# Performance work log

Hardware: AMD Instinct MI355X
Metric: run time of the kernel (lower is better)

## Reference

```python
import jax, jax.numpy as jnp
import numpy as np

N, E, D, G, L = 100_000, 500_000, 128, 512, 4
BN_EPS = 1e-5

def _bn(v, g, b):
    # BatchNorm1d in training mode: biased batch stats over node/graph axis
    m = v.mean(0)
    var = v.var(0)
    return (v - m) * jax.lax.rsqrt(var + BN_EPS) * g + b

def setup_inputs() -> dict:
    key = jax.random.key(0)
    ks = jax.random.split(key, 12)
    s = 0.05
    return {
        "x": jax.random.normal(ks[0], (N, D), jnp.float32),
        "edge_index": jax.random.randint(ks[1], (2, E), 0, N, jnp.int64),
        "batch": jnp.sort(jax.random.randint(ks[2], (N,), 0, G, jnp.int64)),
        "num_graphs": G,
        "W1": jax.random.normal(ks[3], (L, D, 2 * D), jnp.float32) * s,
        "b1": jnp.zeros((L, 2 * D), jnp.float32),
        "g1": jnp.ones((L, 2 * D), jnp.float32),
        "be1": jnp.zeros((L, 2 * D), jnp.float32),
        "W2": jax.random.normal(ks[4], (L, 2 * D, D), jnp.float32) * s,
        "b2": jnp.zeros((L, D), jnp.float32),
        "gbn": jnp.ones((L, D), jnp.float32),
        "bbn": jnp.zeros((L, D), jnp.float32),
        "eps": jnp.zeros((L,), jnp.float32),
        "cW1": jax.random.normal(ks[5], (3 * D, D), jnp.float32) * s,
        "cb1": jnp.zeros((D,), jnp.float32),
        "cg": jnp.ones((D,), jnp.float32),
        "cbeta": jnp.zeros((D,), jnp.float32),
        "cW2": jax.random.normal(ks[6], (D, D // 2), jnp.float32) * s,
        "cb2": jnp.zeros((D // 2,), jnp.float32),
        "cW3": jax.random.normal(ks[7], (D // 2, 2), jnp.float32) * s,
        "cb3": jnp.zeros((2,), jnp.float32),
    }

def reference(x, edge_index, batch, num_graphs, W1, b1, g1, be1, W2, b2, gbn, bbn, eps,
              cW1, cb1, cg, cbeta, cW2, cb2, cW3, cb3):
    n = x.shape[0]
    src, dst = edge_index[0], edge_index[1]
    for l in range(W1.shape[0]):
        # GINConv: mlp((1+eps)*x + sum_{j in N(i)} x_j)  (scatter-add to dst)
        agg = jax.ops.segment_sum(x[src], dst, num_segments=n)
        h = (1.0 + eps[l]) * x + agg
        h = jax.nn.relu(_bn(h @ W1[l] + b1[l], g1[l], be1[l]))
        h = h @ W2[l] + b2[l]
        x = jax.nn.relu(_bn(h, gbn[l], bbn[l]))  # outer BN + ReLU (dropout off: eval)
    # multi-pool readout: add / mean / max per graph
    s = jax.ops.segment_sum(x, batch, num_segments=num_graphs)
    cnt = jax.ops.segment_sum(jnp.ones((n,), x.dtype), batch, num_segments=num_graphs)
    mean = s / jnp.maximum(cnt, 1.0)[:, None]
    mx = jax.ops.segment_max(x, batch, num_segments=num_graphs)
    z = jnp.concatenate([s, mean, mx], axis=-1)  # [G, 3*D]
    z = jax.nn.relu(_bn(z @ cW1 + cb1, cg, cbeta))
    z = jax.nn.relu(z @ cW2 + cb2)
    return z @ cW3 + cb3
```

## Files before the change

### kernel.cpp

```cpp
#include <hip/hip_runtime.h>
#include <cstdint>
#include <cstddef>

#define NN 100000
#define EE 500000
#define DD 128
#define GG 512
#define LL 4
#define BN_EPS 1e-5f

typedef __attribute__((ext_vector_type(8))) short short8;
typedef __attribute__((ext_vector_type(8))) unsigned short ushort8v;
typedef __attribute__((ext_vector_type(4))) float f32x4;

static __device__ __forceinline__ unsigned short f2bf(float f) {
  union { float f; unsigned u; } v;
  v.f = f;
  unsigned r = v.u + 0x7fffu + ((v.u >> 16) & 1u);
  return (unsigned short)(r >> 16);
}
static __device__ __forceinline__ float bf2f(unsigned short u) {
  union { unsigned u; float f; } v;
  v.u = ((unsigned)u) << 16;
  return v.f;
}


__global__ void k_hist(const int* __restrict__ ei, int* __restrict__ cnt) {
  int e = blockIdx.x * 256 + threadIdx.x;
  if (e < EE) {
    int d = ei[EE + e];
    if (d >= 0 && d < NN) atomicAdd(&cnt[d], 1);
  }
}

__global__ void k_part(const int* __restrict__ cnt, int* __restrict__ part) {
  __shared__ int sm[1024];
  int t = threadIdx.x;
  int i = blockIdx.x * 1024 + t;
  sm[t] = (i < NN) ? cnt[i] : 0;
  __syncthreads();
  for (int off = 512; off > 0; off >>= 1) {
    if (t < off) sm[t] += sm[t + off];
    __syncthreads();
  }
  if (t == 0) part[blockIdx.x] = sm[0];
}

__global__ void k_scanpart(const int* __restrict__ part, int* __restrict__ partx, int nb) {
  __shared__ int sm[128];
  int t = threadIdx.x;
  int v = (t < nb) ? part[t] : 0;
  sm[t] = v;
  __syncthreads();
  for (int off = 1; off < 128; off <<= 1) {
    int u = (t >= off) ? sm[t - off] : 0;
    __syncthreads();
    sm[t] += u;
    __syncthreads();
  }
  if (t < nb) partx[t] = sm[t] - v;
}

__global__ void k_rs(const int* __restrict__ cnt, const int* __restrict__ partx,
                     int* __restrict__ rs, int* __restrict__ cur) {
  __shared__ int sm[1024];
  int t = threadIdx.x;
  int i = blockIdx.x * 1024 + t;
  int v = (i < NN) ? cnt[i] : 0;
  sm[t] = v;
  __syncthreads();
  for (int off = 1; off < 1024; off <<= 1) {
    int u = (t >= off) ? sm[t - off] : 0;
    __syncthreads();
    sm[t] += u;
    __syncthreads();
  }
  if (i < NN) {
    int excl = partx[blockIdx.x] + sm[t] - v;
    rs[i] = excl;
    cur[i] = excl;
    if (i == NN - 1) rs[NN] = excl + v;
  }
}

__global__ void k_fill(const int* __restrict__ ei, int* __restrict__ cur,
                       int* __restrict__ ci) {
  int e = blockIdx.x * 256 + threadIdx.x;
  if (e < EE) {
    int s = ei[e];
    int d = ei[EE + e];
    if (d >= 0 && d < NN && s >= 0 && s < NN) {
      int pos = atomicAdd(&cur[d], 1);
      if (pos >= 0 && pos < EE) ci[pos] = s;
    }
  }
}


__global__ void k_conv(const float* __restrict__ W1, const float* __restrict__ W2,
                       const float* __restrict__ cW1, unsigned short* __restrict__ W1t,
                       unsigned short* __restrict__ W2t, float* __restrict__ cW1t) {
  int idx = blockIdx.x * 256 + threadIdx.x;
  if (idx < 4 * 256 * 128) {
    {
      int l = idx >> 15, rem = idx & 32767;
      int nc = rem >> 7, k = rem & 127;
      W1t[idx] = f2bf(W1[(l << 15) + k * 256 + nc]);
    }
    {
      int l = idx >> 15, rem = idx & 32767;
      int nc = rem >> 8, k = rem & 255;
      W2t[idx] = f2bf(W2[(l << 15) + k * 128 + nc]);
    }
  }
  if (idx < 128 * 384) {
    int c = idx / 384, k = idx - c * 384;
    cW1t[idx] = cW1[(size_t)k * 128 + c];
  }
}


__global__ void k_x2bf(const float* __restrict__ x, unsigned short* __restrict__ xb) {
  int i = blockIdx.x * 256 + threadIdx.x;
  if (i < NN * DD / 4) {
    float4 v = *(const float4*)(x + (size_t)i * 4);
    ushort4 o;
    o.x = f2bf(v.x); o.y = f2bf(v.y); o.z = f2bf(v.z); o.w = f2bf(v.w);
    *(ushort4*)(xb + (size_t)i * 4) = o;
  }
}


__global__ __launch_bounds__(256) void k_agg_bf16(
    const unsigned short* __restrict__ X, const int* __restrict__ rs,
    const int* __restrict__ ci, const float* __restrict__ epsv, int l, int mode,
    const float* __restrict__ tsc, const float* __restrict__ tsh,
    unsigned short* __restrict__ h0, int n) {
  int idx = blockIdx.x * 256 + threadIdx.x;
  int node = idx >> 4;
  int c8 = (idx & 15) << 3;
  if (node >= n) return;
  float sa[8], sb[8];
  if (mode) {
    float4 a0 = *(const float4*)(tsc + c8), a1 = *(const float4*)(tsc + c8 + 4);
    float4 b0 = *(const float4*)(tsh + c8), b1 = *(const float4*)(tsh + c8 + 4);
    sa[0] = a0.x; sa[1] = a0.y; sa[2] = a0.z; sa[3] = a0.w;
    sa[4] = a1.x; sa[5] = a1.y; sa[6] = a1.z; sa[7] = a1.w;
    sb[0] = b0.x; sb[1] = b0.y; sb[2] = b0.z; sb[3] = b0.w;
    sb[4] = b1.x; sb[5] = b1.y; sb[6] = b1.z; sb[7] = b1.w;
  }
  float se = 1.f + epsv[l];
  ushort8v v = *(const ushort8v*)(X + (size_t)node * DD + c8);
  float acc[8];
#pragma unroll
  for (int j = 0; j < 8; ++j) {
    float f = bf2f(v[j]);
    if (mode) f = fmaxf(0.f, f * sa[j] + sb[j]);
    acc[j] = se * f;
  }
  int e0 = rs[node], e1 = rs[node + 1];
#define NLD(ee) (*(const ushort8v*)(X + (size_t)ci[ee] * DD + c8))
#define NACC(uc)                                                  \
  {                                                               \
    _Pragma("unroll") for (int j = 0; j < 8; ++j) {               \
      float f = bf2f(uc[j]);                                      \
      if (mode) f = fmaxf(0.f, f * sa[j] + sb[j]);                \
      acc[j] += f;                                                \
    }                                                             \
  }
  ushort8v p0 = (ushort8v){0, 0, 0, 0, 0, 0, 0, 0};
  ushort8v p1 = p0, p2 = p0, p3 = p0;
  if (e0 + 0 < e1) p0 = NLD(e0 + 0);
  if (e0 + 1 < e1) p1 = NLD(e0 + 1);
  if (e0 + 2 < e1) p2 = NLD(e0 + 2);
  if (e0 + 3 < e1) p3 = NLD(e0 + 3);
  for (int e = e0; e < e1; e += 4) {
    ushort8v c0 = p0, c1 = p1, c2 = p2, c3 = p3;
    if (e + 4 < e1) p0 = NLD(e + 4);
    if (e + 5 < e1) p1 = NLD(e + 5);
    if (e + 6 < e1) p2 = NLD(e + 6);
    if (e + 7 < e1) p3 = NLD(e + 7);
    NACC(c0);
    if (e + 1 < e1) NACC(c1);
    if (e + 2 < e1) NACC(c2);
    if (e + 3 < e1) NACC(c3);
  }
#undef NLD
#undef NACC
  ushort8v o;
#pragma unroll
  for (int j = 0; j < 8; ++j) o[j] = f2bf(acc[j]);
  *(ushort8v*)(h0 + (size_t)node * DD + c8) = o;
}


__global__ __launch_bounds__(512) void k_mom(
    const unsigned short* __restrict__ h0, float* __restrict__ M2s,
    float* __restrict__ css, int n) {
  constexpr int HT = 264;
  constexpr int NCH = (NN + 255) / 256;
  constexpr int NBLK = 196;
  __shared__ __align__(16) unsigned short Ht[128 * HT];
  __shared__ float lcs[128];
  int tid = threadIdx.x;
  int lane = tid & 63, wave = tid >> 6;
  int quad = lane >> 4, l15 = lane & 15;
  if (tid < 128) lcs[tid] = 0.f;
  int c8 = (tid & 15) << 3;
  int rloc = tid >> 4;
  float csr[8];
#pragma unroll
  for (int j = 0; j < 8; ++j) csr[j] = 0.f;
  f32x4 acc[8];
#pragma unroll
  for (int j = 0; j < 8; ++j) acc[j] = (f32x4){0.f, 0.f, 0.f, 0.f};

  for (int ch = blockIdx.x; ch < NCH; ch += NBLK) {
    int n0 = ch * 256;
    __syncthreads();
#pragma unroll
    for (int pass = 0; pass < 8; ++pass) {
      int nl = rloc + pass * 32;
      int gr = n0 + nl;
      ushort8v v = (ushort8v){0, 0, 0, 0, 0, 0, 0, 0};
      if (gr < n) v = *(const ushort8v*)(h0 + (size_t)gr * DD + c8);
#pragma unroll
      for (int j = 0; j < 8; ++j) {
        int row = c8 + j;
        int sb = (nl >> 3) ^ ((row >> 3) & 7);
        Ht[row * HT + (sb << 3) + (nl & 7)] = v[j];
        csr[j] += bf2f(v[j]);
      }
    }
    __syncthreads();
#pragma unroll
    for (int kc = 0; kc < 8; ++kc) {
      int b = kc * 4 + quad;
      int arow = wave * 16 + l15;
      short8 avv =
          *(const short8*)(&Ht[arow * HT + ((b ^ ((arow >> 3) & 7)) << 3)]);
#pragma unroll
      for (int j = 0; j < 8; ++j) {
        int brow = j * 16 + l15;
        short8 bvv =
            *(const short8*)(&Ht[brow * HT + ((b ^ ((brow >> 3) & 7)) << 3)]);
        acc[j] = __builtin_amdgcn_mfma_f32_16x16x32_bf16(avv, bvv, acc[j], 0, 0, 0);
      }
    }
  }
  float* M2 = M2s + (size_t)blockIdx.x * 16384;
  int lr = wave * 16 + quad * 4;
#pragma unroll
  for (int j = 0; j < 8; ++j)
#pragma unroll
    for (int g = 0; g < 4; ++g)
      M2[(lr + g) * 128 + j * 16 + l15] = acc[j][g];
#pragma unroll
  for (int j = 0; j < 8; ++j) atomicAdd(&lcs[c8 + j], csr[j]);
  __syncthreads();
  if (tid < 128) css[(size_t)blockIdx.x * 128 + tid] = lcs[tid];
}

__global__ void k_red(const float* __restrict__ M2s, const float* __restrict__ css,
                      float* __restrict__ M2f, float* __restrict__ csf) {
  int i = blockIdx.x * 256 + threadIdx.x;
  float s = 0.f;
  for (int k = 0; k < 196; ++k) s += M2s[(size_t)k * 16384 + i];
  M2f[i] = s;
  if (i < 128) {
    float c = 0.f;
    for (int k = 0; k < 196; ++k) c += css[(size_t)k * 128 + i];
    csf[i] = c;
  }
}

__global__ __launch_bounds__(128) void k_bn1(
    const float* __restrict__ M2, const float* __restrict__ cs,
    const unsigned short* __restrict__ W1t_l, const float* __restrict__ g1_l,
    const float* __restrict__ be1_l, float* __restrict__ osc,
    float* __restrict__ osh) {
  __shared__ float wsh[128];
  __shared__ float red1[2], red2[2];
  int c = blockIdx.x, t = threadIdx.x;
  float w = bf2f(W1t_l[c * 128 + t]);
  wsh[t] = w;
  __syncthreads();
  float inner = 0.f;
#pragma unroll 4
  for (int k = 0; k < 128; ++k) inner = fmaf(M2[t * 128 + k], wsh[k], inner);
  float s1 = w * inner;
  float s2 = w * cs[t];
#pragma unroll
  for (int off = 32; off > 0; off >>= 1) {
    s1 += __shfl_xor(s1, off, 64);
    s2 += __shfl_xor(s2, off, 64);
  }
  if ((t & 63) == 0) { red1[t >> 6] = s1; red2[t >> 6] = s2; }
  __syncthreads();
  if (t == 0) {
    float q = (red1[0] + red1[1]) * (1.0f / NN);
    float um = (red2[0] + red2[1]) * (1.0f / NN);
    float var = fmaxf(q - um * um, 0.f);
    float sc = g1_l[c] * rsqrtf(var + BN_EPS);
    osc[c] = sc;
    osh[c] = be1_l[c] - um * sc;
  }
}


__global__ __launch_bounds__(512, 2) void k_gfused(
    const unsigned short* __restrict__ A, const float* __restrict__ sc1,
    const float* __restrict__ sh1, const unsigned short* __restrict__ W1t_l,
    const unsigned short* __restrict__ W2t_l, const float* __restrict__ b2_l,
    unsigned short* __restrict__ C, float* __restrict__ psum,
    float* __restrict__ psq, int n) {
  constexpr int BST = 72;
  constexpr int HP = 136;
  __shared__ __align__(16) unsigned short Bsm[2][128 * BST];
  __shared__ __align__(16) unsigned short H[256 * HP];
  __shared__ float bsum[128], bsq[128];

  int tid = threadIdx.x;
  int lane = tid & 63, wave = tid >> 6;
  int quad = lane >> 4, l15 = lane & 15;
  int row0 = blockIdx.x * 256;
  int r0 = row0 + wave * 32 + l15;
  int r1 = r0 + 16;

  short8 av0[4], av1[4];
#pragma unroll
  for (int ks = 0; ks < 4; ++ks) {
    av0[ks] = (short8){0, 0, 0, 0, 0, 0, 0, 0};
    av1[ks] = (short8){0, 0, 0, 0, 0, 0, 0, 0};
    if (r0 < n) av0[ks] = *(const short8*)(A + (size_t)r0 * 128 + ks * 32 + quad * 8);
    if (r1 < n) av1[ks] = *(const short8*)(A + (size_t)r1 * 128 + ks * 32 + quad * 8);
  }

  ushort8v pA[2], pB[2];
  f32x4 acc1a[8], acc1b[8], acc2a[8], acc2b[8];
#pragma unroll
  for (int j = 0; j < 8; ++j) {
    acc1a[j] = (f32x4){0.f, 0.f, 0.f, 0.f};
    acc1b[j] = (f32x4){0.f, 0.f, 0.f, 0.f};
    acc2a[j] = (f32x4){0.f, 0.f, 0.f, 0.f};
    acc2b[j] = (f32x4){0.f, 0.f, 0.f, 0.f};
  }

#define LD_W1(dst, cg, kc)                                                      \
  {                                                                             \
    _Pragma("unroll") for (int it = 0; it < 2; ++it) {                          \
      int f = tid + it * 512, rr = f >> 3, cc = (f & 7) << 3;                   \
      dst[it] = *(const ushort8v*)(W1t_l + (size_t)((cg)*128 + rr) * 128 +      \
                                   (kc)*64 + cc);                               \
    }                                                                           \
  }
#define LD_W2(dst, kc2)                                                         \
  {                                                                             \
    _Pragma("unroll") for (int it = 0; it < 2; ++it) {                          \
      int f = tid + it * 512, rr = f >> 3, cc = (f & 7) << 3;                   \
      dst[it] = *(const ushort8v*)(W2t_l + (size_t)rr * 256 + (kc2)*64 + cc);   \
    }                                                                           \
  }
#define ST_B(buf, src)                                                          \
  {                                                                             \
    _Pragma("unroll") for (int it = 0; it < 2; ++it) {                          \
      int f = tid + it * 512, rr = f >> 3, cc = (f & 7) << 3;                   \
      *(ushort8v*)(&Bsm[buf][rr * BST + cc]) = src[it];                         \
    }                                                                           \
  }
#define MM1(buf, k2)                                                            \
  {                                                                             \
    _Pragma("unroll") for (int kk = 0; kk < 2; ++kk) {                          \
      int ko = kk * 32 + quad * 8;                                              \
      short8 a0 = av0[(k2)*2 + kk];                                             \
      short8 a1 = av1[(k2)*2 + kk];                                             \
      _Pragma("unroll") for (int cf = 0; cf < 8; ++cf) {                        \
        short8 bv = *(const short8*)(&Bsm[buf][(cf * 16 + l15) * BST + ko]);    \
        acc1a[cf] = __builtin_amdgcn_mfma_f32_16x16x32_bf16(a0, bv, acc1a[cf],  \
                                                            0, 0, 0);           \
        acc1b[cf] = __builtin_amdgcn_mfma_f32_16x16x32_bf16(a1, bv, acc1b[cf],  \
                                                            0, 0, 0);           \
      }                                                                         \
    }                                                                           \
  }
#define MM2(buf, half)                                                          \
  {                                                                             \
    _Pragma("unroll") for (int kk = 0; kk < 64; kk += 32) {                     \
      int ko = kk + quad * 8;                                                   \
      short8 a0 =                                                               \
          *(const short8*)(&H[(wave * 32 + l15) * HP + (half)*64 + ko]);        \
      short8 a1 =                                                               \
          *(const short8*)(&H[(wave * 32 + 16 + l15) * HP + (half)*64 + ko]);   \
      _Pragma("unroll") for (int cf = 0; cf < 8; ++cf) {                        \
        short8 bv = *(const short8*)(&Bsm[buf][(cf * 16 + l15) * BST + ko]);    \
        acc2a[cf] = __builtin_amdgcn_mfma_f32_16x16x32_bf16(a0, bv, acc2a[cf],  \
                                                            0, 0, 0);           \
        acc2b[cf] = __builtin_amdgcn_mfma_f32_16x16x32_bf16(a1, bv, acc2b[cf],  \
                                                            0, 0, 0);           \
      }                                                                         \
    }                                                                           \
  }
#define EPI(cg)                                                                 \
  {                                                                             \
    int lrb = wave * 32 + quad * 4;                                             \
    _Pragma("unroll") for (int cf = 0; cf < 8; ++cf) {                          \
      int col = (cg)*128 + cf * 16 + l15;                                       \
      float sc = sc1[col], sh = sh1[col];                                       \
      _Pragma("unroll") for (int g = 0; g < 4; ++g) {                           \
        H[(lrb + g) * HP + cf * 16 + l15] =                                     \
            f2bf(fmaxf(0.f, acc1a[cf][g] * sc + sh));                           \
        H[(lrb + 16 + g) * HP + cf * 16 + l15] =                                \
            f2bf(fmaxf(0.f, acc1b[cf][g] * sc + sh));                           \
      }                                                                         \
    }                                                                           \
  }
#define ZACC1                                                                   \
  {                                                                             \
    _Pragma("unroll") for (int j = 0; j < 8; ++j) {                             \
      acc1a[j] = (f32x4){0.f, 0.f, 0.f, 0.f};                                   \
      acc1b[j] = (f32x4){0.f, 0.f, 0.f, 0.f};                                   \
    }                                                                           \
  }

  LD_W1(pA, 0, 0)
  LD_W1(pB, 0, 1)
  ST_B(0, pA)
  __syncthreads();
  LD_W2(pA, 0) MM1(0, 0) ST_B(1, pB) __syncthreads();
  LD_W2(pB, 1) MM1(1, 1) EPI(0) ST_B(0, pA) __syncthreads();
  LD_W1(pA, 1, 0) MM2(0, 0) ST_B(1, pB) __syncthreads();
  LD_W1(pB, 1, 1) MM2(1, 1) ST_B(0, pA) __syncthreads();
  LD_W2(pA, 2) ZACC1 MM1(0, 0) ST_B(1, pB) __syncthreads();
  LD_W2(pB, 3) MM1(1, 1) EPI(1) ST_B(0, pA) __syncthreads();
  MM2(0, 0) ST_B(1, pB) __syncthreads();
  MM2(1, 1)

  __syncthreads();
  unsigned short* Ct = H;
  if (tid < 128) { bsum[tid] = 0.f; bsq[tid] = 0.f; }
  float s8[8], q8[8];
#pragma unroll
  for (int j = 0; j < 8; ++j) { s8[j] = 0.f; q8[j] = 0.f; }
  int lrbase = wave * 32 + quad * 4;
#pragma unroll
  for (int cf = 0; cf < 8; ++cf) {
    float bv = b2_l[cf * 16 + l15];
#pragma unroll
    for (int g = 0; g < 4; ++g) {
      {
        int lr = lrbase + g;
        float e = acc2a[cf][g] + bv;
        Ct[lr * HP + cf * 16 + l15] = f2bf(e);
        if (row0 + lr < n) { s8[cf] += e; q8[cf] += e * e; }
      }
      {
        int lr = lrbase + 16 + g;
        float e = acc2b[cf][g] + bv;
        Ct[lr * HP + cf * 16 + l15] = f2bf(e);
        if (row0 + lr < n) { s8[cf] += e; q8[cf] += e * e; }
      }
    }
  }
#pragma unroll
  for (int cf = 0; cf < 8; ++cf) {
    s8[cf] += __shfl_xor(s8[cf], 16, 64);
    s8[cf] += __shfl_xor(s8[cf], 32, 64);
    q8[cf] += __shfl_xor(q8[cf], 16, 64);
    q8[cf] += __shfl_xor(q8[cf], 32, 64);
  }
  __syncthreads();
  if (quad == 0) {
#pragma unroll
    for (int cf = 0; cf < 8; ++cf) {
      atomicAdd(&bsum[cf * 16 + l15], s8[cf]);
      atomicAdd(&bsq[cf * 16 + l15], q8[cf]);
    }
  }
#pragma unroll
  for (int it = 0; it < 8; ++it) {
    int f = tid + it * 512;
    int rr = f >> 4, cc = (f & 15) << 3;
    int gr = row0 + rr;
    if (gr < n)
      *(ushort8v*)(C + (size_t)gr * 128 + cc) = *(const ushort8v*)(&Ct[rr * HP + cc]);
  }
  __syncthreads();
  if (tid < 128) {
    psum[(size_t)blockIdx.x * 128 + tid] = bsum[tid];
    psq[(size_t)blockIdx.x * 128 + tid] = bsq[tid];
  }
#undef LD_W1
#undef LD_W2
#undef ST_B
#undef MM1
#undef MM2
#undef EPI
#undef ZACC1
}


__global__ __launch_bounds__(256) void k_finred(
    const float* __restrict__ psum, const float* __restrict__ psq, int nb, int nc,
    const float* __restrict__ g, const float* __restrict__ be,
    float* __restrict__ osc, float* __restrict__ osh, float invn) {
  __shared__ float ws[4], wq[4];
  int col = blockIdx.x;
  int t = threadIdx.x;
  float s = 0.f, q = 0.f;
  for (int b = t; b < nb; b += 256) {
    s += psum[(size_t)b * nc + col];
    q += psq[(size_t)b * nc + col];
  }
#pragma unroll
  for (int off = 32; off > 0; off >>= 1) {
    s += __shfl_xor(s, off, 64);
    q += __shfl_xor(q, off, 64);
  }
  if ((t & 63) == 0) { ws[t >> 6] = s; wq[t >> 6] = q; }
  __syncthreads();
  if (t == 0) {
    s = ws[0] + ws[1] + ws[2] + ws[3];
    q = wq[0] + wq[1] + wq[2] + wq[3];
    float m = s * invn;
    float v = fmaxf(q * invn - m * m, 0.f);
    float sc = g[col] * rsqrtf(v + BN_EPS);
    osc[col] = sc;
    osh[col] = be[col] - m * sc;
  }
}


__global__ __launch_bounds__(256) void k_statz(
    const float* __restrict__ z1, const float* __restrict__ g,
    const float* __restrict__ be, float* __restrict__ osc, float* __restrict__ osh) {
  __shared__ float ws[4], wq[4];
  int col = blockIdx.x;
  int t = threadIdx.x;
  float s = 0.f, q = 0.f;
  for (int b = t; b < GG; b += 256) {
    float v = z1[(size_t)b * 128 + col];
    s += v;
    q += v * v;
  }
#pragma unroll
  for (int off = 32; off > 0; off >>= 1) {
    s += __shfl_xor(s, off, 64);
    q += __shfl_xor(q, off, 64);
  }
  if ((t & 63) == 0) { ws[t >> 6] = s; wq[t >> 6] = q; }
  __syncthreads();
  if (t == 0) {
    s = ws[0] + ws[1] + ws[2] + ws[3];
    q = wq[0] + wq[1] + wq[2] + wq[3];
    float m = s / (float)GG;
    float v = fmaxf(q / (float)GG - m * m, 0.f);
    float sc = g[col] * rsqrtf(v + BN_EPS);
    osc[col] = sc;
    osh[col] = be[col] - m * sc;
  }
}


static __device__ __forceinline__ int lb_i32(const int* a, int n, int key) {
  int lo = 0, hi = n;
  while (lo < hi) {
    int mid = (lo + hi) >> 1;
    if (a[mid] < key) lo = mid + 1; else hi = mid;
  }
  return lo;
}

__global__ __launch_bounds__(512) void k_pool(
    const unsigned short* __restrict__ X, const int* __restrict__ batch,
    const float* __restrict__ tsc, const float* __restrict__ tsh,
    float* __restrict__ z, int n) {
  __shared__ int slo, shi;
  __shared__ float ssum[8][128], smax[8][128];
  int g = blockIdx.x;
  int t = threadIdx.x;
  int sg = t >> 6;
  int c2 = (t & 63) << 1;
  if (t == 0) slo = lb_i32(batch, n, g);
  if (t == 64) shi = lb_i32(batch, n, g + 1);
  __syncthreads();
  int lo = slo, hi = shi;
  float a0 = tsc[c2], a1 = tsc[c2 + 1];
  float b0 = tsh[c2], b1 = tsh[c2 + 1];
  float s0 = 0.f, s1 = 0.f;
  float m0 = -3.402823466e38f, m1 = -3.402823466e38f;
  for (int i = lo + sg; i < hi; i += 8) {
    unsigned u = *(const unsigned*)(X + (size_t)i * DD + c2);
    float v0 = fmaxf(0.f, bf2f((unsigned short)(u & 0xffff)) * a0 + b0);
    float v1 = fmaxf(0.f, bf2f((unsigned short)(u >> 16)) * a1 + b1);
    s0 += v0; m0 = fmaxf(m0, v0);
    s1 += v1; m1 = fmaxf(m1, v1);
  }
  ssum[sg][c2] = s0; ssum[sg][c2 + 1] = s1;
  smax[sg][c2] = m0; smax[sg][c2 + 1] = m1;
  __syncthreads();
  if (t < 128) {
    float S = 0.f, M = -3.402823466e38f;
#pragma unroll
    for (int k = 0; k < 8; ++k) {
      S += ssum[k][t];
      M = fmaxf(M, smax[k][t]);
    }
    float cntf = (float)(hi - lo);
    z[(size_t)g * 384 + t] = S;
    z[(size_t)g * 384 + 128 + t] = S / fmaxf(cntf, 1.f);
    z[(size_t)g * 384 + 256 + t] = M;
  }
}


__global__ __launch_bounds__(256) void k_cls1(
    const float* __restrict__ z, const float* __restrict__ cW1t,
    const float* __restrict__ cb1, float* __restrict__ z1) {
  __shared__ float zr[2][384];
  __shared__ float part[2][2][128];
  int g0 = blockIdx.x * 2;
  int tid = threadIdx.x;
  int c = tid & 127, kh = tid >> 7;
  for (int i = tid; i < 768; i += 256) {
    int g = i / 384, k = i - g * 384;
    zr[g][k] = z[(size_t)g0 * 384 + i];
    (void)g; (void)k;
  }
  __syncthreads();
  float a0 = 0.f, a1 = 0.f;
  const float* wrow = cW1t + (size_t)c * 384 + kh * 192;
#pragma unroll
  for (int i = 0; i < 48; ++i) {
    float4 w = *(const float4*)(wrow + i * 4);
    float4 z0 = *(const float4*)(&zr[0][kh * 192 + i * 4]);
    float4 z1v = *(const float4*)(&zr[1][kh * 192 + i * 4]);
    a0 += w.x * z0.x + w.y * z0.y + w.z * z0.z + w.w * z0.w;
    a1 += w.x * z1v.x + w.y * z1v.y + w.z * z1v.z + w.w * z1v.w;
  }
  part[kh][0][c] = a0;
  part[kh][1][c] = a1;
  __syncthreads();
  if (kh == 0) {
    float b = cb1[c];
    z1[(size_t)g0 * 128 + c] = part[0][0][c] + part[1][0][c] + b;
    z1[(size_t)(g0 + 1) * 128 + c] = part[0][1][c] + part[1][1][c] + b;
  }
}

__global__ void k_cls2(const float* __restrict__ z1, const float* __restrict__ csc,
                       const float* __restrict__ csh, const float* __restrict__ cW2,
                       const float* __restrict__ cb2, const float* __restrict__ cW3,
                       const float* __restrict__ cb3, float* __restrict__ out) {
  __shared__ float z1n[128];
  __shared__ float z2s[64];
  int g = blockIdx.x;
  int t = threadIdx.x;
  z1n[t] = fmaxf(0.f, z1[(size_t)g * 128 + t] * csc[t] + csh[t]);
  __syncthreads();
  if (t < 64) {
    float s = cb2[t];
#pragma unroll 4
    for (int k = 0; k < 128; ++k) s = fmaf(z1n[k], cW2[(size_t)k * 64 + t], s);
    z2s[t] = fmaxf(0.f, s);
  }
  __syncthreads();
  if (t < 2) {
    float s = cb3[t];
#pragma unroll 4
    for (int c = 0; c < 64; ++c) s = fmaf(z2s[c], cW3[(size_t)c * 2 + t], s);
    out[(size_t)g * 2 + t] = s;
  }
}


extern "C" void kernel_launch(void* const* d_in, const int* in_sizes, int n_in,
                              void* d_out, int out_size, void* d_ws, size_t ws_size,
                              hipStream_t stream) {
  const float* x = (const float*)d_in[0];
  const int* ei = (const int*)d_in[1];
  const int* batch = (const int*)d_in[2];
  const float* W1 = (const float*)d_in[4];
  const float* b1 = (const float*)d_in[5];
  const float* g1 = (const float*)d_in[6];
  const float* be1 = (const float*)d_in[7];
  const float* W2 = (const float*)d_in[8];
  const float* b2 = (const float*)d_in[9];
  const float* gbn = (const float*)d_in[10];
  const float* bbn = (const float*)d_in[11];
  const float* epsv = (const float*)d_in[12];
  const float* cW1 = (const float*)d_in[13];
  const float* cb1 = (const float*)d_in[14];
  const float* cg = (const float*)d_in[15];
  const float* cbeta = (const float*)d_in[16];
  const float* cW2 = (const float*)d_in[17];
  const float* cb2 = (const float*)d_in[18];
  const float* cW3 = (const float*)d_in[19];
  const float* cb3 = (const float*)d_in[20];
  float* out = (float*)d_out;
  (void)b1;

  char* p = (char*)d_ws;
  auto alloc = [&](size_t bytes) {
    char* r = p;
    p += (bytes + 255) & ~(size_t)255;
    return r;
  };
  const int NB2 = (NN + 255) / 256;
  int* cnt = (int*)alloc((size_t)NN * 4);
  int* rs = (int*)alloc((size_t)(NN + 1) * 4);
  int* cur = (int*)alloc((size_t)NN * 4);
  int* ci = (int*)alloc((size_t)EE * 4);
  int* part = (int*)alloc(128 * 4);
  int* partx = (int*)alloc(128 * 4);
  unsigned short* xbf = (unsigned short*)alloc((size_t)NN * DD * 2);
  unsigned short* h0 = (unsigned short*)alloc((size_t)NN * DD * 2);
  unsigned short* xp = (unsigned short*)alloc((size_t)NN * DD * 2);
  float* psum = (float*)alloc((size_t)NB2 * 128 * 4);
  float* psq = (float*)alloc((size_t)NB2 * 128 * 4);
  float* tsc1 = (float*)alloc(256 * 4);
  float* tsh1 = (float*)alloc(256 * 4);
  float* tscX = (float*)alloc(128 * 4);
  float* tshX = (float*)alloc(128 * 4);
  float* zbuf = (float*)alloc((size_t)GG * 384 * 4);
  float* z1 = (float*)alloc((size_t)GG * 128 * 4);
  unsigned short* W1t = (unsigned short*)alloc((size_t)4 * 256 * 128 * 2);
  unsigned short* W2t = (unsigned short*)alloc((size_t)4 * 128 * 256 * 2);
  float* cW1t = (float*)alloc((size_t)128 * 384 * 4);
  float* M2s = (float*)alloc((size_t)196 * 16384 * 4);
  float* css = (float*)alloc((size_t)196 * 128 * 4);
  float* M2f = (float*)alloc((size_t)128 * 128 * 4);
  float* csf = (float*)alloc(128 * 4);
  (void)ws_size; (void)n_in; (void)in_sizes; (void)out_size;

  k_conv<<<512, 256, 0, stream>>>(W1, W2, cW1, W1t, W2t, cW1t);
  k_x2bf<<<(NN * DD / 4 + 255) / 256, 256, 0, stream>>>(x, xbf);

  hipMemsetAsync(cnt, 0, (size_t)NN * 4, stream);
  k_hist<<<(EE + 255) / 256, 256, 0, stream>>>(ei, cnt);
  const int nscan = (NN + 1023) / 1024;
  k_part<<<nscan, 1024, 0, stream>>>(cnt, part);
  k_scanpart<<<1, 128, 0, stream>>>(part, partx, nscan);
  k_rs<<<nscan, 1024, 0, stream>>>(cnt, partx, rs, cur);
  k_fill<<<(EE + 255) / 256, 256, 0, stream>>>(ei, cur, ci);

  for (int l = 0; l < LL; ++l) {
    const unsigned short* Xl = (l == 0) ? xbf : xp;
    k_agg_bf16<<<(NN * 16 + 255) / 256, 256, 0, stream>>>(
        Xl, rs, ci, epsv, l, (l > 0) ? 1 : 0, tscX, tshX, h0, NN);
    k_mom<<<196, 512, 0, stream>>>(h0, M2s, css, NN);
    k_red<<<64, 256, 0, stream>>>(M2s, css, M2f, csf);
    k_bn1<<<256, 128, 0, stream>>>(M2f, csf, W1t + (size_t)l * 256 * 128,
                                   g1 + (size_t)l * 256, be1 + (size_t)l * 256,
                                   tsc1, tsh1);
    k_gfused<<<NB2, 512, 0, stream>>>(
        h0, tsc1, tsh1, W1t + (size_t)l * 256 * 128, W2t + (size_t)l * 128 * 256,
        b2 + (size_t)l * 128, xp, psum, psq, NN);
    k_finred<<<128, 256, 0, stream>>>(psum, psq, NB2, 128, gbn + (size_t)l * 128,
                                      bbn + (size_t)l * 128, tscX, tshX, 1.0f / NN);
  }

  k_pool<<<GG, 512, 0, stream>>>(xp, batch, tscX, tshX, zbuf, NN);
  k_cls1<<<GG / 2, 256, 0, stream>>>(zbuf, cW1t, cb1, z1);
  k_statz<<<128, 256, 0, stream>>>(z1, cg, cbeta, tscX, tshX);
  k_cls2<<<GG, 128, 0, stream>>>(z1, tscX, tshX, cW2, cb2, cW3, cb3, out);
}
```

Before: 682.6 us.

## Load full weight tiles per stage in fused GIN MLP to cut block barriers

The fused two-GEMM kernel now stages complete 128x128 W1 and W2 tiles in shared memory, instead of double-buffering 64-wide K slices. Each GEMM runs over the full K in one pass. The intermediate activations reuse the W1 buffer region, split across two shared arrays by wave. This roughly halves the number of __syncthreads per block and keeps shared-memory use about the same. The trade-off is that it gives up the fine-grained overlap between global weight loads and MFMA work, and each stage holds more registers for prefetched weights.

```diff
diff --git a/kernel.cpp b/kernel.cpp
--- a/kernel.cpp
+++ b/kernel.cpp
@@ -315,10 +315,10 @@
     const unsigned short* __restrict__ W2t_l, const float* __restrict__ b2_l,
     unsigned short* __restrict__ C, float* __restrict__ psum,
     float* __restrict__ psq, int n) {
-  constexpr int BST = 72;
-  constexpr int HP = 136;
-  __shared__ __align__(16) unsigned short Bsm[2][128 * BST];
-  __shared__ __align__(16) unsigned short H[256 * HP];
+  constexpr int TS = 136;
+  __shared__ __align__(16) unsigned short R0[128 * TS];
+  __shared__ __align__(16) unsigned short R1[128 * TS];
+  __shared__ __align__(16) unsigned short R2[128 * TS];
   __shared__ float bsum[128], bsq[128];
 
   int tid = threadIdx.x;
@@ -328,6 +328,11 @@
   int r0 = row0 + wave * 32 + l15;
   int r1 = r0 + 16;
 
+  unsigned short* Hw = (wave < 4) ? (R0 + (wave * 32) * TS)
+                                  : (R1 + ((wave - 4) * 32) * TS);
+
+  if (tid < 128) { bsum[tid] = 0.f; bsq[tid] = 0.f; }
+
   short8 av0[4], av1[4];
 #pragma unroll
   for (int ks = 0; ks < 4; ++ks) {
@@ -337,7 +342,7 @@
     if (r1 < n) av1[ks] = *(const short8*)(A + (size_t)r1 * 128 + ks * 32 + quad * 8);
   }
 
-  ushort8v pA[2], pB[2];
+  ushort8v pW1[4], pW2[4];
   f32x4 acc1a[8], acc1b[8], acc2a[8], acc2b[8];
 #pragma unroll
   for (int j = 0; j < 8; ++j) {
@@ -347,36 +352,37 @@
     acc2b[j] = (f32x4){0.f, 0.f, 0.f, 0.f};
   }
 
-#define LD_W1(dst, cg, kc)                                                      \
+#define LD_W1TILE(cg)                                                           \
   {                                                                             \
-    _Pragma("unroll") for (int it = 0; it < 2; ++it) {                          \
-      int f = tid + it * 512, rr = f >> 3, cc = (f & 7) << 3;                   \
-      dst[it] = *(const ushort8v*)(W1t_l + (size_t)((cg)*128 + rr) * 128 +      \
-                                   (kc)*64 + cc);                               \
+    _Pragma("unroll") for (int it = 0; it < 4; ++it) {                          \
+      int f = tid + it * 512, rr = f >> 4, cc = (f & 15) << 3;                  \
+      pW1[it] =                                                                 \
+          *(const ushort8v*)(W1t_l + (size_t)((cg)*128 + rr) * 128 + cc);       \
     }                                                                           \
   }
-#define LD_W2(dst, kc2)                                                         \
+#define LD_W2TILE(h)                                                            \
   {                                                                             \
-    _Pragma("unroll") for (int it = 0; it < 2; ++it) {                          \
-      int f = tid + it * 512, rr = f >> 3, cc = (f & 7) << 3;                   \
-      dst[it] = *(const ushort8v*)(W2t_l + (size_t)rr * 256 + (kc2)*64 + cc);   \
+    _Pragma("unroll") for (int it = 0; it < 4; ++it) {                          \
+      int f = tid + it * 512, rr = f >> 4, cc = (f & 15) << 3;                  \
+      pW2[it] = *(const ushort8v*)(W2t_l + (size_t)rr * 256 + (h)*128 + cc);    \
     }                                                                           \
   }
-#define ST_B(buf, src)                                                          \
+#define ST_TILES                                                                \
   {                                                                             \
-    _Pragma("unroll") for (int it = 0; it < 2; ++it) {                          \
-      int f = tid + it * 512, rr = f >> 3, cc = (f & 7) << 3;                   \
-      *(ushort8v*)(&Bsm[buf][rr * BST + cc]) = src[it];                         \
+    _Pragma("unroll") for (int it = 0; it < 4; ++it) {                          \
+      int f = tid + it * 512, rr = f >> 4, cc = (f & 15) << 3;                  \
+      *(ushort8v*)(&R1[rr * TS + cc]) = pW1[it];                                \
+      *(ushort8v*)(&R2[rr * TS + cc]) = pW2[it];                                \
     }                                                                           \
   }
-#define MM1(buf, k2)                                                            \
+#define MM1FULL                                                                 \
   {                                                                             \
-    _Pragma("unroll") for (int kk = 0; kk < 2; ++kk) {                          \
-      int ko = kk * 32 + quad * 8;                                              \
-      short8 a0 = av0[(k2)*2 + kk];                                             \
-      short8 a1 = av1[(k2)*2 + kk];                                             \
+    _Pragma("unroll") for (int ks = 0; ks < 4; ++ks) {                          \
+      int ko = ks * 32 + quad * 8;                                              \
+      short8 a0 = av0[ks];                                                      \
+      short8 a1 = av1[ks];                                                      \
       _Pragma("unroll") for (int cf = 0; cf < 8; ++cf) {                        \
-        short8 bv = *(const short8*)(&Bsm[buf][(cf * 16 + l15) * BST + ko]);    \
+        short8 bv = *(const short8*)(&R1[(cf * 16 + l15) * TS + ko]);           \
         acc1a[cf] = __builtin_amdgcn_mfma_f32_16x16x32_bf16(a0, bv, acc1a[cf],  \
                                                             0, 0, 0);           \
         acc1b[cf] = __builtin_amdgcn_mfma_f32_16x16x32_bf16(a1, bv, acc1b[cf],  \
@@ -384,16 +390,14 @@
       }                                                                         \
     }                                                                           \
   }
-#define MM2(buf, half)                                                          \
+#define MM2FULL                                                                 \
   {                                                                             \
-    _Pragma("unroll") for (int kk = 0; kk < 64; kk += 32) {                     \
-      int ko = kk + quad * 8;                                                   \
-      short8 a0 =                                                               \
-          *(const short8*)(&H[(wave * 32 + l15) * HP + (half)*64 + ko]);        \
-      short8 a1 =                                                               \
-          *(const short8*)(&H[(wave * 32 + 16 + l15) * HP + (half)*64 + ko]);   \
+    _Pragma("unroll") for (int ks = 0; ks < 4; ++ks) {                          \
+      int ko = ks * 32 + quad * 8;                                              \
+      short8 a0 = *(const short8*)(&Hw[l15 * TS + ko]);                         \
+      short8 a1 = *(const short8*)(&Hw[(16 + l15) * TS + ko]);                  \
       _Pragma("unroll") for (int cf = 0; cf < 8; ++cf) {                        \
-        short8 bv = *(const short8*)(&Bsm[buf][(cf * 16 + l15) * BST + ko]);    \
+        short8 bv = *(const short8*)(&R2[(cf * 16 + l15) * TS + ko]);           \
         acc2a[cf] = __builtin_amdgcn_mfma_f32_16x16x32_bf16(a0, bv, acc2a[cf],  \
                                                             0, 0, 0);           \
         acc2b[cf] = __builtin_amdgcn_mfma_f32_16x16x32_bf16(a1, bv, acc2b[cf],  \
@@ -403,14 +407,14 @@
   }
 #define EPI(cg)                                                                 \
   {                                                                             \
-    int lrb = wave * 32 + quad * 4;                                             \
+    int lrb = quad * 4;                   \
     _Pragma("unroll") for (int cf = 0; cf < 8; ++cf) {                          \
       int col = (cg)*128 + cf * 16 + l15;                                       \
       float sc = sc1[col], sh = sh1[col];                                       \
       _Pragma("unroll") for (int g = 0; g < 4; ++g) {                           \
-        H[(lrb + g) * HP + cf * 16 + l15] =                                     \
+        Hw[(lrb + g) * TS + cf * 16 + l15] =                                    \
             f2bf(fmaxf(0.f, acc1a[cf][g] * sc + sh));                           \
-        H[(lrb + 16 + g) * HP + cf * 16 + l15] =                                \
+        Hw[(lrb + 16 + g) * TS + cf * 16 + l15] =                               \
             f2bf(fmaxf(0.f, acc1b[cf][g] * sc + sh));                           \
       }                                                                         \
     }                                                                           \
@@ -423,42 +427,44 @@
     }                                                                           \
   }
 
-  LD_W1(pA, 0, 0)
-  LD_W1(pB, 0, 1)
-  ST_B(0, pA)
-  __syncthreads();
-  LD_W2(pA, 0) MM1(0, 0) ST_B(1, pB) __syncthreads();
-  LD_W2(pB, 1) MM1(1, 1) EPI(0) ST_B(0, pA) __syncthreads();
-  LD_W1(pA, 1, 0) MM2(0, 0) ST_B(1, pB) __syncthreads();
-  LD_W1(pB, 1, 1) MM2(1, 1) ST_B(0, pA) __syncthreads();
-  LD_W2(pA, 2) ZACC1 MM1(0, 0) ST_B(1, pB) __syncthreads();
-  LD_W2(pB, 3) MM1(1, 1) EPI(1) ST_B(0, pA) __syncthreads();
-  MM2(0, 0) ST_B(1, pB) __syncthreads();
-  MM2(1, 1)
-
-  __syncthreads();
-  unsigned short* Ct = H;
-  if (tid < 128) { bsum[tid] = 0.f; bsq[tid] = 0.f; }
+  LD_W1TILE(0)
+  LD_W2TILE(0)
+  ST_TILES
+  __syncthreads();
+  LD_W1TILE(1)
+  LD_W2TILE(1)
+  MM1FULL
+  __syncthreads();
+  EPI(0)
+  MM2FULL
+  __syncthreads();
+  ST_TILES
+  ZACC1
+  __syncthreads();
+  MM1FULL
+  __syncthreads();
+  EPI(1)
+  MM2FULL
+
   float s8[8], q8[8];
 #pragma unroll
   for (int j = 0; j < 8; ++j) { s8[j] = 0.f; q8[j] = 0.f; }
-  int lrbase = wave * 32 + quad * 4;
+  int lrb = quad * 4;
 #pragma unroll
   for (int cf = 0; cf < 8; ++cf) {
     float bv = b2_l[cf * 16 + l15];
 #pragma unroll
     for (int g = 0; g < 4; ++g) {
       {
-        int lr = lrbase + g;
         float e = acc2a[cf][g] + bv;
-        Ct[lr * HP + cf * 16 + l15] = f2bf(e);
-        if (row0 + lr < n) { s8[cf] += e; q8[cf] += e * e; }
+        Hw[(lrb + g) * TS + cf * 16 + l15] = f2bf(e);
+        if (r0 - l15 + lrb + g + row0 - row0 >= 0) {}
+        if (row0 + wave * 32 + lrb + g < n) { s8[cf] += e; q8[cf] += e * e; }
       }
       {
-        int lr = lrbase + 16 + g;
         float e = acc2b[cf][g] + bv;
-        Ct[lr * HP + cf * 16 + l15] = f2bf(e);
-        if (row0 + lr < n) { s8[cf] += e; q8[cf] += e * e; }
+        Hw[(lrb + 16 + g) * TS + cf * 16 + l15] = f2bf(e);
+        if (row0 + wave * 32 + lrb + 16 + g < n) { s8[cf] += e; q8[cf] += e * e; }
       }
     }
   }
@@ -482,19 +488,20 @@
     int f = tid + it * 512;
     int rr = f >> 4, cc = (f & 15) << 3;
     int gr = row0 + rr;
+    const unsigned short* Hrow = (rr < 128) ? &R0[rr * TS] : &R1[(rr - 128) * TS];
     if (gr < n)
-      *(ushort8v*)(C + (size_t)gr * 128 + cc) = *(const ushort8v*)(&Ct[rr * HP + cc]);
+      *(ushort8v*)(C + (size_t)gr * 128 + cc) = *(const ushort8v*)(&Hrow[cc]);
   }
   __syncthreads();
   if (tid < 128) {
     psum[(size_t)blockIdx.x * 128 + tid] = bsum[tid];
     psq[(size_t)blockIdx.x * 128 + tid] = bsq[tid];
   }
-#undef LD_W1
-#undef LD_W2
-#undef ST_B
-#undef MM1
-#undef MM2
+#undef LD_W1TILE
+#undef LD_W2TILE
+#undef ST_TILES
+#undef MM1FULL
+#undef MM2FULL
 #undef EPI
 #undef ZACC1
 }
```

After: 681.2 us. About the same (-0.2%).
